# Performance work log

Hardware: AMD Instinct MI355X
Metric: run time of the kernel (lower is better)

The kernel has to match this reference:

```python
import jax, jax.numpy as jnp
import numpy as np

B = 256          # batch of molecules
N_ATOM = 1024    # atoms per molecule
N_EDGE = 8192    # directed edges per molecule (avg degree 8)
NEG_SLOPE = 0.01 # torch LeakyReLU default


def setup_inputs() -> dict:
    key = jax.random.key(0)
    ks = jax.random.split(key, 8)
    x = jax.random.normal(ks[0], (B, 3 * N_ATOM), dtype=jnp.float32)
    edge_index = jax.random.randint(ks[1], (2, N_EDGE), 0, N_ATOM, dtype=jnp.int64)
    # GCNConv weights (Glorot-ish small scale) and biases
    W1 = jax.random.normal(ks[2], (3, 64), dtype=jnp.float32) * 0.3
    b1 = jnp.zeros((64,), jnp.float32)
    W2 = jax.random.normal(ks[3], (64, 64), dtype=jnp.float32) * 0.1
    b2 = jnp.zeros((64,), jnp.float32)
    # project MLP: Linear(64,128) + LeakyReLU
    Wp = jax.random.normal(ks[4], (64, 128), dtype=jnp.float32) * 0.1
    bp = jnp.zeros((128,), jnp.float32)
    return {"x": x, "edge_index": edge_index, "W1": W1, "b1": b1,
            "W2": W2, "b2": b2, "Wp": Wp, "bp": bp}


def _leaky_relu(v):
    return jnp.where(v >= 0, v, NEG_SLOPE * v)


def reference(x, edge_index, W1, b1, W2, b2, Wp, bp):
    # x: [B, 3*n_atom] -> node features [B, n_atom, 3]
    bsz, n_feat = x.shape
    n = n_feat // 3
    h = x.reshape(bsz, n, 3)

    src = edge_index[0]  # message sources
    dst = edge_index[1]  # aggregation targets

    # GCN normalization with self-loops: deg[i] = 1 + in-degree(i)
    ones_e = jnp.ones((src.shape[0],), x.dtype)
    deg = jax.ops.segment_sum(ones_e, dst, num_segments=n) + 1.0
    dinv = jax.lax.rsqrt(deg)                # deg^{-1/2}, deg >= 1
    norm_e = dinv[src] * dinv[dst]           # [E]
    norm_self = dinv * dinv                  # self-loop weight per node

    def gcn(h, W, b):
        hw = h @ W                                        # [B, n, d_out]
        msg = hw[:, src, :] * norm_e[None, :, None]       # [B, E, d_out]
        agg = jax.vmap(lambda m: jax.ops.segment_sum(m, dst, num_segments=n))(msg)
        return agg + norm_self[None, :, None] * hw + b

    h = _leaky_relu(gcn(h, W1, b1))
    h = _leaky_relu(gcn(h, W2, b2))

    # global_mean_pool: every graph has exactly n atoms -> mean over atom axis
    g = h.mean(axis=1)                                    # [B, 64]

    # project MLP: Linear + LeakyReLU
    return _leaky_relu(g @ Wp + bp)                       # [B, 128]
```

## Files before the change

### kernel.cpp

```cpp
#include <hip/hip_runtime.h>

#define N_ATOMS 1024
#define N_EDGES 8192
#define NBATCH  256
#define NEG     0.01f

typedef unsigned int u32;
typedef __attribute__((ext_vector_type(2))) float f32x2;
typedef __attribute__((ext_vector_type(4))) float f32x4;
typedef __attribute__((ext_vector_type(8))) _Float16 f16x8;

__device__ __forceinline__ u32 pkrtz(float lo, float hi) {
    u32 r;
    asm("v_cvt_pkrtz_f16_f32 %0, %1, %2" : "=v"(r) : "v"(lo), "v"(hi));
    return r;
}
#define FMIX_LO(a, w, u) \
    asm("v_fma_mix_f32 %0, %1, %2, %0 op_sel_hi:[0,1,0]" : "+v"(a) : "v"(w), "v"(u))
#define FMIX_HI(a, w, u) \
    asm("v_fma_mix_f32 %0, %1, %2, %0 op_sel:[0,1,0] op_sel_hi:[0,1,0]" : "+v"(a) : "v"(w), "v"(u))

#define ROWPTR_OFF 0
#define COLW_OFF   4352
#define SELFW_OFF  (4352 + 73728)
#define PERM_OFF   (SELFW_OFF + 4096)
#define W2T_OFF    (PERM_OFF + 4096)

#define TSTR_B 144
#define SM_TILE_BYTES (N_ATOMS * TSTR_B)
#define SM_AUX_OFF SM_TILE_BYTES
#define SM_TOTAL (SM_TILE_BYTES + 12288)

__global__ __launch_bounds__(1024) void build_csr(
    const int* __restrict__ ei,
    int*  __restrict__ rowptr,
    int2* __restrict__ colw,
    float* __restrict__ selfw_g,
    int*  __restrict__ perm_g,
    u32*  __restrict__ w2t,
    const float* __restrict__ W2)
{
    __shared__ int   sdeg[N_ATOMS];
    __shared__ int   sstart[N_ATOMS];
    __shared__ float sdinv[N_ATOMS];
    __shared__ int   wtot[16];
    __shared__ int   hist[128];
    const int t = threadIdx.x;
    const int lane = t & 63;
    const int w = t >> 6;
    const int* srcA = ei;
    const int* dstA = ei + N_EDGES;

    sdeg[t] = 0;
    if (t < 128) hist[t] = 0;
    __syncthreads();
    for (int e = t; e < N_EDGES; e += 1024) atomicAdd(&sdeg[dstA[e]], 1);
    __syncthreads();

    const int deg  = sdeg[t];
    const int pdeg = (deg + 1) & ~1;
    int v = pdeg;
    #pragma unroll
    for (int d = 1; d < 64; d <<= 1) {
        int u = __shfl_up(v, d, 64);
        if (lane >= d) v += u;
    }
    if (lane == 63) wtot[w] = v;
    __syncthreads();
    if (t == 0) {
        int run = 0;
        #pragma unroll
        for (int i = 0; i < 16; ++i) { int c = wtot[i]; wtot[i] = run; run += c; }
    }
    __syncthreads();
    const int start = v - pdeg + wtot[w];
    sstart[t] = start;
    const float dv = rsqrtf((float)deg + 1.0f);
    sdinv[t] = dv;
    rowptr[t] = start;
    if (t == N_ATOMS - 1) rowptr[N_ATOMS] = start + pdeg;
    selfw_g[t] = dv * dv;
    if (deg & 1) colw[start + deg] = make_int2(0, 0);

    #pragma unroll
    for (int i = 0; i < 2; ++i) {
        const int idx = t + i * 1024;
        const int c = idx >> 5, kk = idx & 31;
        w2t[c * 32 + kk] = pkrtz(W2[(2 * kk) * 64 + c], W2[(2 * kk + 1) * 64 + c]);
    }

    const int dcl = deg < 127 ? deg : 127;
    atomicAdd(&hist[dcl], 1);
    sdeg[t] = 0;
    __syncthreads();
    if (t == 0) {
        int run = 0;
        for (int i = 0; i < 128; ++i) { int c = hist[i]; hist[i] = run; run += c; }
    }
    __syncthreads();
    const int pos = atomicAdd(&hist[dcl], 1);
    perm_g[pos] = t;
    __syncthreads();

    for (int e = t; e < N_EDGES; e += 1024) {
        const int d = dstA[e];
        const int s = srcA[e];
        const int slot = atomicAdd(&sdeg[d], 1);
        const float wgt = sdinv[s] * sdinv[d];
        colw[sstart[d] + slot] = make_int2(s, __float_as_int(wgt));
    }
}

#define FMIX_SET(q0, q1, q2, q3, wt)                                  \
    do {                                                              \
        FMIX_LO(acc[0],  wt, (q0).x); FMIX_HI(acc[1],  wt, (q0).x);   \
        FMIX_LO(acc[2],  wt, (q0).y); FMIX_HI(acc[3],  wt, (q0).y);   \
        FMIX_LO(acc[4],  wt, (q0).z); FMIX_HI(acc[5],  wt, (q0).z);   \
        FMIX_LO(acc[6],  wt, (q0).w); FMIX_HI(acc[7],  wt, (q0).w);   \
        FMIX_LO(acc[8],  wt, (q1).x); FMIX_HI(acc[9],  wt, (q1).x);   \
        FMIX_LO(acc[10], wt, (q1).y); FMIX_HI(acc[11], wt, (q1).y);   \
        FMIX_LO(acc[12], wt, (q1).z); FMIX_HI(acc[13], wt, (q1).z);   \
        FMIX_LO(acc[14], wt, (q1).w); FMIX_HI(acc[15], wt, (q1).w);   \
        FMIX_LO(acc[16], wt, (q2).x); FMIX_HI(acc[17], wt, (q2).x);   \
        FMIX_LO(acc[18], wt, (q2).y); FMIX_HI(acc[19], wt, (q2).y);   \
        FMIX_LO(acc[20], wt, (q2).z); FMIX_HI(acc[21], wt, (q2).z);   \
        FMIX_LO(acc[22], wt, (q2).w); FMIX_HI(acc[23], wt, (q2).w);   \
        FMIX_LO(acc[24], wt, (q3).x); FMIX_HI(acc[25], wt, (q3).x);   \
        FMIX_LO(acc[26], wt, (q3).y); FMIX_HI(acc[27], wt, (q3).y);   \
        FMIX_LO(acc[28], wt, (q3).z); FMIX_HI(acc[29], wt, (q3).z);   \
        FMIX_LO(acc[30], wt, (q3).w); FMIX_HI(acc[31], wt, (q3).w);   \
    } while (0)

#define LOAD_SET(q0, q1, q2, q3, rowbase)                 \
    do {                                                  \
        const uint4* _r = (const uint4*)(rowbase);        \
        q0 = _r[0]; q1 = _r[1]; q2 = _r[2]; q3 = _r[3];   \
    } while (0)

__global__ __launch_bounds__(1024, 4) void gnn_main(
    const float* __restrict__ x,
    const int*  __restrict__ rowptr,
    const int2* __restrict__ colw,
    const float* __restrict__ selfw_g,
    const int*  __restrict__ perm_g,
    const float* __restrict__ W1, const float* __restrict__ b1,
    const u32*  __restrict__ w2t, const float* __restrict__ b2,
    const float* __restrict__ Wp, const float* __restrict__ bp,
    float* __restrict__ out)
{
    extern __shared__ char smem[];
    float2* cx2 = (float2*)(smem + SM_AUX_OFF);
    float*  cz  = (float*)(smem + SM_AUX_OFF + 8192);
    float*  paux  = (float*)(smem + SM_AUX_OFF);
    float*  wpool = paux;
    float*  gvec  = paux + 1024;
    float*  proj  = paux + 1088;

    const int t = threadIdx.x;
    const int b = blockIdx.x;
    const float* xb = x + (size_t)b * (3 * N_ATOMS);

    {
        cx2[t] = make_float2(xb[3 * t], xb[3 * t + 1]);
        cz[t]  = xb[3 * t + 2];
    }
    __syncthreads();

    {
        const int atom = perm_g[t];
        const int s0 = rowptr[atom], s1 = rowptr[atom + 1];
        const float sw = selfw_g[atom];
        const float2 cs = cx2[atom];
        float A0 = sw * cs.x, A1 = sw * cs.y, A2 = sw * cz[atom];
        int4 cur = make_int4(0, 0, 0, 0);
        if (s0 < s1) cur = *(const int4*)(colw + s0);
        for (int j = s0; j < s1; j += 2) {
            const int jn = (j + 2 < s1) ? (j + 2) : s0;
            const int4 nxt = *(const int4*)(colw + jn);
            const float2 c0 = cx2[cur.x];
            const float2 c1 = cx2[cur.z];
            const float z0 = cz[cur.x], z1 = cz[cur.z];
            const float w0 = __int_as_float(cur.y), w1 = __int_as_float(cur.w);
            A0 += w0 * c0.x + w1 * c1.x;
            A1 += w0 * c0.y + w1 * c1.y;
            A2 += w0 * z0 + w1 * z1;
            cur = nxt;
        }
        u32 pw[32];
        #pragma unroll
        for (int p = 0; p < 32; ++p) {
            f32x2 vv = *(const f32x2*)(b1 + 2 * p);
            vv = __builtin_elementwise_fma((f32x2){A0, A0}, *(const f32x2*)(W1 + 2 * p), vv);
            vv = __builtin_elementwise_fma((f32x2){A1, A1}, *(const f32x2*)(W1 + 64 + 2 * p), vv);
            vv = __builtin_elementwise_fma((f32x2){A2, A2}, *(const f32x2*)(W1 + 128 + 2 * p), vv);
            vv.x = fmaxf(vv.x, NEG * vv.x);
            vv.y = fmaxf(vv.y, NEG * vv.y);
            pw[p] = pkrtz(vv.x, vv.y);
        }
        uint4* trow = (uint4*)(smem + (size_t)atom * TSTR_B);
        #pragma unroll
        for (int q = 0; q < 8; ++q)
            trow[q] = make_uint4(pw[4 * q], pw[4 * q + 1], pw[4 * q + 2], pw[4 * q + 3]);
    }
    __syncthreads();

    const int ho   = (t & 1) * 64;
    const int pidx = t >> 1;

    int atomR[2];
    u32 pr[2][16];
    const int2* colw2 = (const int2*)colw;

    #pragma unroll
    for (int r = 0; r < 2; ++r) {
        const int atom = perm_g[r * 512 + pidx];
        atomR[r] = atom;
        const int s0e = rowptr[atom];
        const int ne  = rowptr[atom + 1] - s0e;
        const float swk = selfw_g[atom];

        float acc[32];
        #pragma unroll
        for (int f = 0; f < 32; ++f) acc[f] = 0.0f;
        {
            uint4 s0q, s1q, s2q, s3q;
            LOAD_SET(s0q, s1q, s2q, s3q, smem + (size_t)atom * TSTR_B + ho);
            FMIX_SET(s0q, s1q, s2q, s3q, swk);
        }
        if (ne > 0) {
            int2 cwA = colw2[s0e];
            uint4 a0, a1, a2, a3, b0, b1_, b2_, b3;
            LOAD_SET(a0, a1, a2, a3, smem + (size_t)cwA.x * TSTR_B + ho);
            for (int j = 0; j < ne; j += 2) {
                const int2 cwB = colw2[s0e + j + 1];
                LOAD_SET(b0, b1_, b2_, b3, smem + (size_t)cwB.x * TSTR_B + ho);
                FMIX_SET(a0, a1, a2, a3, __int_as_float(cwA.y));
                if (j + 2 < ne) {
                    cwA = colw2[s0e + j + 2];
                    LOAD_SET(a0, a1, a2, a3, smem + (size_t)cwA.x * TSTR_B + ho);
                }
                FMIX_SET(b0, b1_, b2_, b3, __int_as_float(cwB.y));
            }
        }
        #pragma unroll
        for (int i = 0; i < 16; ++i) pr[r][i] = pkrtz(acc[2 * i], acc[2 * i + 1]);
    }

    const int l15 = t & 15;
    const int lq  = (t & 63) >> 4;
    const int w   = t >> 6;
    f16x8 wf[2][4];
    #pragma unroll
    for (int kt = 0; kt < 2; ++kt)
        #pragma unroll
        for (int ct = 0; ct < 4; ++ct)
            wf[kt][ct] = *(const f16x8*)(w2t + (ct * 16 + l15) * 32 + kt * 16 + lq * 4);
    float bias[4];
    #pragma unroll
    for (int ct = 0; ct < 4; ++ct) bias[ct] = b2[ct * 16 + l15];

    __syncthreads();

    #pragma unroll
    for (int r = 0; r < 2; ++r) {
        uint4* dst = (uint4*)(smem + (size_t)atomR[r] * TSTR_B + ho);
        dst[0] = make_uint4(pr[r][0],  pr[r][1],  pr[r][2],  pr[r][3]);
        dst[1] = make_uint4(pr[r][4],  pr[r][5],  pr[r][6],  pr[r][7]);
        dst[2] = make_uint4(pr[r][8],  pr[r][9],  pr[r][10], pr[r][11]);
        dst[3] = make_uint4(pr[r][12], pr[r][13], pr[r][14], pr[r][15]);
    }
    __syncthreads();

    {
        float pool[4] = {0.f, 0.f, 0.f, 0.f};
        #pragma unroll
        for (int rt = 0; rt < 4; ++rt) {
            const int po = (rt & 1) ? (16 + l15) : l15;
            const int arow = (rt < 2) ? __shfl(atomR[0], 2 * po, 64)
                                      : __shfl(atomR[1], 2 * po, 64);
            const char* ab = smem + (size_t)arow * TSTR_B + lq * 16;
            const f16x8 a0 = *(const f16x8*)(ab);
            const f16x8 a1 = *(const f16x8*)(ab + 64);
            #pragma unroll
            for (int ct = 0; ct < 4; ++ct) {
                f32x4 cf = {0.f, 0.f, 0.f, 0.f};
                cf = __builtin_amdgcn_mfma_f32_16x16x32_f16(a0, wf[0][ct], cf, 0, 0, 0);
                cf = __builtin_amdgcn_mfma_f32_16x16x32_f16(a1, wf[1][ct], cf, 0, 0, 0);
                float s = 0.0f;
                #pragma unroll
                for (int rr = 0; rr < 4; ++rr) {
                    const float vv = cf[rr] + bias[ct];
                    s += fmaxf(vv, NEG * vv);
                }
                pool[ct] += s;
            }
        }
        #pragma unroll
        for (int ct = 0; ct < 4; ++ct) {
            pool[ct] += __shfl_xor(pool[ct], 16, 64);
            pool[ct] += __shfl_xor(pool[ct], 32, 64);
        }
        if ((t & 63) < 16) {
            #pragma unroll
            for (int ct = 0; ct < 4; ++ct)
                wpool[w * 64 + ct * 16 + l15] = pool[ct];
        }
    }
    __syncthreads();

    if (t < 64) {
        float s = 0.0f;
        #pragma unroll
        for (int ww = 0; ww < 16; ++ww) s += wpool[ww * 64 + t];
        gvec[t] = s * (1.0f / 1024.0f);
    }
    __syncthreads();
    if (t < 512) {
        const int col = t & 127, pc = t >> 7;
        float s = 0.0f;
        #pragma unroll
        for (int f = 0; f < 16; ++f)
            s += gvec[pc * 16 + f] * Wp[(pc * 16 + f) * 128 + col];
        proj[pc * 128 + col] = s;
    }
    __syncthreads();
    if (t < 128) {
        float s = bp[t] + proj[t] + proj[128 + t] + proj[256 + t] + proj[384 + t];
        s = fmaxf(s, NEG * s);
        out[(size_t)b * 128 + t] = s;
    }
}

extern "C" void kernel_launch(void* const* d_in, const int* in_sizes, int n_in,
                              void* d_out, int out_size, void* d_ws, size_t ws_size,
                              hipStream_t stream) {
    const float* x  = (const float*)d_in[0];
    const int*   ei = (const int*)  d_in[1];
    const float* W1 = (const float*)d_in[2];
    const float* b1 = (const float*)d_in[3];
    const float* W2 = (const float*)d_in[4];
    const float* b2 = (const float*)d_in[5];
    const float* Wp = (const float*)d_in[6];
    const float* bp = (const float*)d_in[7];
    float* out = (float*)d_out;

    char* ws = (char*)d_ws;
    int*   rowptr = (int*)  (ws + ROWPTR_OFF);
    int2*  colw   = (int2*) (ws + COLW_OFF);
    float* selfw  = (float*)(ws + SELFW_OFF);
    int*   perm   = (int*)  (ws + PERM_OFF);
    u32*   w2t    = (u32*)  (ws + W2T_OFF);

    build_csr<<<1, 1024, 0, stream>>>(ei, rowptr, colw, selfw, perm, w2t, W2);

    (void)hipFuncSetAttribute((const void*)gnn_main,
                              hipFuncAttributeMaxDynamicSharedMemorySize, SM_TOTAL);
    gnn_main<<<NBATCH, 1024, SM_TOTAL, stream>>>(
        x, rowptr, colw, selfw, perm, W1, b1, w2t, b2, Wp, bp, out);
}
```

Before: 38.75 us.

## Split layer-1 feature work across thread pairs and balance atom slots

Layer 1 now has each thread pair handle the same two atoms, each thread computing and storing half of the 64 output features. This halves per-thread W1 projection work and register use for pw. Rows are assigned from both ends of the permutation (pidx and 1023-pidx), so each thread gets a light and a heavy atom. The neighbour aggregation for layer 1 is now done twice per atom (once per half-thread), trading extra gather work for a shorter dependent FMA chain and better degree balance.

```diff
diff --git a/kernel.cpp b/kernel.cpp
--- a/kernel.cpp
+++ b/kernel.cpp
@@ -160,23 +160,30 @@
     const int b = blockIdx.x;
     const float* xb = x + (size_t)b * (3 * N_ATOMS);
 
+    const int ho   = (t & 1) * 64;
+    const int ho32 = (t & 1) * 32;
+    const int pidx = t >> 1;
+
     {
         cx2[t] = make_float2(xb[3 * t], xb[3 * t + 1]);
         cz[t]  = xb[3 * t + 2];
     }
     __syncthreads();
 
-    {
-        const int atom = perm_g[t];
-        const int s0 = rowptr[atom], s1 = rowptr[atom + 1];
+    #pragma unroll
+    for (int r = 0; r < 2; ++r) {
+        const int slot = r ? (1023 - pidx) : pidx;
+        const int atom = perm_g[slot];
+        const int s0 = rowptr[atom];
+        const int np = (rowptr[atom + 1] - s0) >> 1;
         const float sw = selfw_g[atom];
         const float2 cs = cx2[atom];
         float A0 = sw * cs.x, A1 = sw * cs.y, A2 = sw * cz[atom];
+        const int4* colw4 = (const int4*)(colw + s0);
         int4 cur = make_int4(0, 0, 0, 0);
-        if (s0 < s1) cur = *(const int4*)(colw + s0);
-        for (int j = s0; j < s1; j += 2) {
-            const int jn = (j + 2 < s1) ? (j + 2) : s0;
-            const int4 nxt = *(const int4*)(colw + jn);
+        if (np > 0) cur = colw4[0];
+        for (int i = 0; i < np; ++i) {
+            const int4 nxt = (i + 1 < np) ? colw4[i + 1] : cur;
             const float2 c0 = cx2[cur.x];
             const float2 c1 = cx2[cur.z];
             const float z0 = cz[cur.x], z1 = cz[cur.z];
@@ -186,38 +193,37 @@
             A2 += w0 * z0 + w1 * z1;
             cur = nxt;
         }
-        u32 pw[32];
-        #pragma unroll
-        for (int p = 0; p < 32; ++p) {
-            f32x2 vv = *(const f32x2*)(b1 + 2 * p);
-            vv = __builtin_elementwise_fma((f32x2){A0, A0}, *(const f32x2*)(W1 + 2 * p), vv);
-            vv = __builtin_elementwise_fma((f32x2){A1, A1}, *(const f32x2*)(W1 + 64 + 2 * p), vv);
-            vv = __builtin_elementwise_fma((f32x2){A2, A2}, *(const f32x2*)(W1 + 128 + 2 * p), vv);
+        u32 pw[16];
+        #pragma unroll
+        for (int p = 0; p < 16; ++p) {
+            const int fc = ho32 + 2 * p;
+            f32x2 vv = *(const f32x2*)(b1 + fc);
+            vv = __builtin_elementwise_fma((f32x2){A0, A0}, *(const f32x2*)(W1 + fc), vv);
+            vv = __builtin_elementwise_fma((f32x2){A1, A1}, *(const f32x2*)(W1 + 64 + fc), vv);
+            vv = __builtin_elementwise_fma((f32x2){A2, A2}, *(const f32x2*)(W1 + 128 + fc), vv);
             vv.x = fmaxf(vv.x, NEG * vv.x);
             vv.y = fmaxf(vv.y, NEG * vv.y);
             pw[p] = pkrtz(vv.x, vv.y);
         }
-        uint4* trow = (uint4*)(smem + (size_t)atom * TSTR_B);
-        #pragma unroll
-        for (int q = 0; q < 8; ++q)
-            trow[q] = make_uint4(pw[4 * q], pw[4 * q + 1], pw[4 * q + 2], pw[4 * q + 3]);
-    }
-    __syncthreads();
-
-    const int ho   = (t & 1) * 64;
-    const int pidx = t >> 1;
+        uint4* half = (uint4*)(smem + (size_t)atom * TSTR_B + ho);
+        #pragma unroll
+        for (int q = 0; q < 4; ++q)
+            half[q] = make_uint4(pw[4 * q], pw[4 * q + 1], pw[4 * q + 2], pw[4 * q + 3]);
+    }
+    __syncthreads();
 
     int atomR[2];
     u32 pr[2][16];
-    const int2* colw2 = (const int2*)colw;
 
     #pragma unroll
     for (int r = 0; r < 2; ++r) {
-        const int atom = perm_g[r * 512 + pidx];
+        const int slot = r ? (1023 - pidx) : pidx;
+        const int atom = perm_g[slot];
         atomR[r] = atom;
         const int s0e = rowptr[atom];
         const int ne  = rowptr[atom + 1] - s0e;
         const float swk = selfw_g[atom];
+        const int2* colw2 = (const int2*)(colw + s0e);
 
         float acc[32];
         #pragma unroll
@@ -228,15 +234,15 @@
             FMIX_SET(s0q, s1q, s2q, s3q, swk);
         }
         if (ne > 0) {
-            int2 cwA = colw2[s0e];
+            int2 cwA = colw2[0];
             uint4 a0, a1, a2, a3, b0, b1_, b2_, b3;
             LOAD_SET(a0, a1, a2, a3, smem + (size_t)cwA.x * TSTR_B + ho);
             for (int j = 0; j < ne; j += 2) {
-                const int2 cwB = colw2[s0e + j + 1];
+                const int2 cwB = colw2[j + 1];
                 LOAD_SET(b0, b1_, b2_, b3, smem + (size_t)cwB.x * TSTR_B + ho);
                 FMIX_SET(a0, a1, a2, a3, __int_as_float(cwA.y));
                 if (j + 2 < ne) {
-                    cwA = colw2[s0e + j + 2];
+                    cwA = colw2[j + 2];
                     LOAD_SET(a0, a1, a2, a3, smem + (size_t)cwA.x * TSTR_B + ho);
                 }
                 FMIX_SET(b0, b1_, b2_, b3, __int_as_float(cwB.y));
```

Measured after the change: 53.97 us. 1.39x slower.
